# Performance work log

Hardware: AMD Instinct MI355X
Metric: run time of the kernel (lower is better)

## Reference

```python
import jax, jax.numpy as jnp
import numpy as np

G = 2            # num_codevector_groups
C = 320          # num_codevectors_per_group
VQ_DIM = 256     # codevector_dim
HID = 512        # conv_dimensions[-1]
TAU = 2.0


def setup_inputs() -> dict:
    key = jax.random.key(0)
    k1, k2, k3, k4 = jax.random.split(key, 4)
    B, S = 16, 2048
    x = jax.random.normal(k1, (B, S, HID), dtype=jnp.float32)
    # iid Gumbel(0,1) noise, same shape as flattened logits [B*S*G, C]
    u = jax.random.uniform(k2, (B * S * G, C), dtype=jnp.float32, minval=1e-6, maxval=1.0 - 1e-6)
    gumbel = -jnp.log(-jnp.log(u))
    Wq = jax.random.normal(k3, (G * C, HID), dtype=jnp.float32) * (1.0 / np.sqrt(HID))
    bq = jnp.zeros((G * C,), dtype=jnp.float32)
    codevectors = jax.random.uniform(k4, (1, G * C, VQ_DIM // G), dtype=jnp.float32)
    return {"x": x, "gumbel": gumbel, "Wq": Wq, "bq": bq, "codevectors": codevectors}


def reference(x, gumbel, Wq, bq, codevectors):
    B, S, H = x.shape
    N = B * S
    logits = jnp.einsum('bsh,gh->bsg', x, Wq) + bq          # [B, S, G*C]
    logits = logits.reshape(N * G, C)

    # hard gumbel-softmax (training path) with straight-through estimator
    y_soft = jax.nn.softmax((logits + gumbel) / TAU, axis=-1)
    idx = jnp.argmax(y_soft, axis=-1)
    y_hard = jax.nn.one_hot(idx, C, dtype=y_soft.dtype)
    probs = y_hard + y_soft - jax.lax.stop_gradient(y_soft)  # [N*G, C]

    # perplexity from plain softmax of logits (no gumbel noise), masked_token_idx=None
    soft_probs = jax.nn.softmax(logits.reshape(N, G, C), axis=-1)
    mean_p = soft_probs.mean(axis=0)                          # [G, C]
    perplexity = jnp.exp(-jnp.sum(mean_p * jnp.log(mean_p + 1e-7), axis=-1)).sum()

    # weighted sum over codes per group == einsum (same math as broadcast*sum in torch)
    cv = codevectors.reshape(G, C, VQ_DIM // G)               # [G, C, d]
    sel = jnp.einsum('ngc,gcd->ngd', probs.reshape(N, G, C), cv)
    selected_codes = sel.reshape(B, S, VQ_DIM)
    return selected_codes, perplexity
```

## Files before the change

### kernel.cpp

```cpp
#include <hip/hip_runtime.h>
#include <hip/hip_fp16.h>

#define HID 512
#define GC  640
#define CC  320
#define GG  2
#define DHALF 128
#define MARGIN 0.004f
#define FB 4

typedef __attribute__((ext_vector_type(8))) _Float16 half8;
typedef __attribute__((ext_vector_type(4))) float float4v;

__device__ __forceinline__ void gload16(const void* g, void* l) {
    __builtin_amdgcn_global_load_lds(
        (const __attribute__((address_space(1))) void*)(unsigned long long)g,
        (__attribute__((address_space(3))) void*)(unsigned)(unsigned long long)l,
        16, 0, 0);
}

__global__ __launch_bounds__(256) void zero_misc(float* meanAcc, int* cnt) {
    for (int i = threadIdx.x; i < GC; i += 256) meanAcc[i] = 0.f;
    if (threadIdx.x < 2) cnt[threadIdx.x] = 0;
}

__global__ __launch_bounds__(256) void convert_f16(
    const float* __restrict__ in, unsigned short* __restrict__ out, int n8)
{
    int i = blockIdx.x * 256 + threadIdx.x;
    if (i >= n8) return;
    const float4* p = (const float4*)in + (size_t)i * 2;
    float4 v0 = p[0], v1 = p[1];
    float f[8] = {v0.x, v0.y, v0.z, v0.w, v1.x, v1.y, v1.z, v1.w};
    unsigned r[4];
#pragma unroll
    for (int j = 0; j < 4; ++j) {
        __half2 hh = __float22half2_rn(make_float2(f[2*j], f[2*j+1]));
        r[j] = __builtin_bit_cast(unsigned, hh);
    }
    uint4 o = {r[0], r[1], r[2], r[3]};
    *(uint4*)(out + (size_t)i * 8) = o;
}

__global__ __launch_bounds__(256) void gemm_f16(
    const unsigned short* __restrict__ Xh,
    const unsigned short* __restrict__ Wh,
    const float* __restrict__ bq,
    float* __restrict__ L)
{
    __shared__ __align__(16) unsigned short As[128 * 32];
    __shared__ __align__(16) unsigned short Bs[128 * 32];
    const int tid  = threadIdx.x;
    const int lane = tid & 63;
    const int wid  = tid >> 6;
    const int wr   = wid >> 1, wc = wid & 1;
    const int brow = blockIdx.x * 128;
    const int bcol = blockIdx.y * 128;

    float4v acc[4][4] = {};

    const int chunk = (wid * 2) * 64 + lane;
    const int rowA0 = (chunk >> 2);
    const int k8A0  = (chunk & 3) * 8;
    const int chunk1 = (wid * 2 + 1) * 64 + lane;
    const int rowA1 = (chunk1 >> 2);
    const int k8A1  = (chunk1 & 3) * 8;

    for (int k0 = 0; k0 < HID; k0 += 32) {
        gload16(Xh + (size_t)(brow + rowA0) * HID + k0 + k8A0, &As[(wid * 2 + 0) * 512]);
        gload16(Xh + (size_t)(brow + rowA1) * HID + k0 + k8A1, &As[(wid * 2 + 1) * 512]);
        gload16(Wh + (size_t)(bcol + rowA0) * HID + k0 + k8A0, &Bs[(wid * 2 + 0) * 512]);
        gload16(Wh + (size_t)(bcol + rowA1) * HID + k0 + k8A1, &Bs[(wid * 2 + 1) * 512]);
        __syncthreads();
        half8 a[4], b[4];
#pragma unroll
        for (int t = 0; t < 4; ++t) {
            a[t] = *(const half8*)(const void*)&As[(wr * 64 + t * 16 + (lane & 15)) * 32 + (lane >> 4) * 8];
            b[t] = *(const half8*)(const void*)&Bs[(wc * 64 + t * 16 + (lane & 15)) * 32 + (lane >> 4) * 8];
        }
#pragma unroll
        for (int mt = 0; mt < 4; ++mt)
#pragma unroll
            for (int nt = 0; nt < 4; ++nt)
                acc[mt][nt] = __builtin_amdgcn_mfma_f32_16x16x32_f16(a[mt], b[nt], acc[mt][nt], 0, 0, 0);
        __syncthreads();
    }
#pragma unroll
    for (int mt = 0; mt < 4; ++mt) {
#pragma unroll
        for (int nt = 0; nt < 4; ++nt) {
            int col = bcol + wc * 64 + nt * 16 + (lane & 15);
            float bias = bq[col];
#pragma unroll
            for (int r = 0; r < 4; ++r) {
                int row = brow + wr * 64 + mt * 16 + (lane >> 4) * 4 + r;
                L[(size_t)row * GC + col] = acc[mt][nt][r] + bias;
            }
        }
    }
}

__global__ __launch_bounds__(512) void postproc(
    const float* __restrict__ L, const float* __restrict__ gum,
    const float* __restrict__ cv, float* __restrict__ out,
    float* __restrict__ meanAcc, int* __restrict__ cnt,
    int* __restrict__ flags0, int* __restrict__ flags1, int tok0)
{
    __shared__ float smean[GC];
    for (int i = threadIdx.x; i < GC; i += 512) smean[i] = 0.f;
    __syncthreads();

    const int lane = threadIdx.x & 63;
    const int wid  = threadIdx.x >> 6;
    const int g    = wid >> 2;
    const int lq   = lane & 15;
    const int tq   = lane >> 4;
    const int c0   = lq * 20;
    int* flagsg = g ? flags1 : flags0;

    float macc[20];
#pragma unroll
    for (int j = 0; j < 20; ++j) macc[j] = 0.f;

    for (int it = 0; it < 4; ++it) {
        const int tloc  = blockIdx.x * 64 + (wid & 3) * 16 + it * 4 + tq;
        const int tglob = tok0 + tloc;
        const float* lrow = L   + (size_t)tloc * GC + g * CC + c0;
        const float* grow = gum + ((size_t)tglob * GG + g) * CC + c0;

        float le[20], ve[20];
#pragma unroll
        for (int jj = 0; jj < 5; ++jj) {
            float4 lv = *(const float4*)(lrow + jj * 4);
            float4 gv = *(const float4*)(grow + jj * 4);
            le[jj*4+0] = lv.x; le[jj*4+1] = lv.y; le[jj*4+2] = lv.z; le[jj*4+3] = lv.w;
            ve[jj*4+0] = lv.x + gv.x; ve[jj*4+1] = lv.y + gv.y;
            ve[jj*4+2] = lv.z + gv.z; ve[jj*4+3] = lv.w + gv.w;
        }
        float s = 0.f;
#pragma unroll
        for (int j = 0; j < 20; ++j) { le[j] = __expf(le[j]); s += le[j]; }
        float b = ve[0]; int bi = c0; float s2 = -3.0e38f;
#pragma unroll
        for (int j = 1; j < 20; ++j) {
            float v = ve[j];
            if (v > b) { s2 = b; b = v; bi = c0 + j; }
            else if (v > s2) s2 = v;
        }
#pragma unroll
        for (int m = 1; m < 16; m <<= 1) {
            float os  = __shfl_xor(s,  m, 64);
            float ob  = __shfl_xor(b,  m, 64);
            int   obi = __shfl_xor(bi, m, 64);
            float os2 = __shfl_xor(s2, m, 64);
            s += os;
            if (ob > b || (ob == b && obi < bi)) { s2 = fmaxf(os2, b); b = ob; bi = obi; }
            else                                 { s2 = fmaxf(s2, ob); }
        }
        float inv = 1.f / s;
#pragma unroll
        for (int j = 0; j < 20; ++j) macc[j] += le[j] * inv;

        if (lq == 0 && (b - s2) < MARGIN) {
            int p = atomicAdd(&cnt[g], 1);
            flagsg[p] = tglob;
        }
        const float* cvp = cv + ((size_t)(g * CC + bi)) * DHALF + lq * 8;
        float4 c0v = *(const float4*)cvp;
        float4 c1v = *(const float4*)(cvp + 4);
        float* op = out + (size_t)tglob * 256 + g * DHALF + lq * 8;
        *(float4*)op       = c0v;
        *(float4*)(op + 4) = c1v;
    }
#pragma unroll
    for (int j = 0; j < 20; ++j) {
        macc[j] += __shfl_xor(macc[j], 16, 64);
        macc[j] += __shfl_xor(macc[j], 32, 64);
    }
    if (lane < 16) {
#pragma unroll
        for (int j = 0; j < 20; ++j)
            atomicAdd(&smean[g * CC + c0 + j], macc[j]);
    }
    __syncthreads();
    for (int i = threadIdx.x; i < GC; i += 512)
        atomicAdd(&meanAcc[i], smean[i]);
}

__global__ __launch_bounds__(320) void fixup(
    const float* __restrict__ X, const float* __restrict__ W,
    const float* __restrict__ bq, const float* __restrict__ gum,
    const float* __restrict__ cv, float* __restrict__ out,
    const int* __restrict__ flags0, const int* __restrict__ flags1,
    const int* __restrict__ cnt)
{
    __shared__ float xs[FB][HID];
    __shared__ float vals[FB][CC];
    __shared__ int stok[FB];
    const int tid = threadIdx.x;
    const int n0 = cnt[0], n1 = cnt[1];
    const int nb0 = (n0 + FB - 1) / FB;
    const int nb1 = (n1 + FB - 1) / FB;

    for (int bb = blockIdx.x; bb < nb0 + nb1; bb += gridDim.x) {
        const int g    = (bb < nb0) ? 0 : 1;
        const int lb   = (bb < nb0) ? bb : bb - nb0;
        const int n    = g ? n1 : n0;
        const int* fl  = g ? flags1 : flags0;
        const int r0   = lb * FB;
        const int nr   = (n - r0 < FB) ? (n - r0) : FB;

        if (tid < FB) {
            int idx = r0 + tid;
            if (idx >= n) idx = n - 1;
            stok[tid] = fl[idx];
        }
        __syncthreads();
        for (int i = tid; i < FB * (HID / 4); i += 320) {
            int r = i >> 7, k4 = i & 127;
            *(float4*)&xs[r][k4 * 4] = *(const float4*)(X + (size_t)stok[r] * HID + k4 * 4);
        }
        __syncthreads();

        {
            const int c = tid;
            if (c < CC) {
                const float* wr = W + (size_t)(g * CC + c) * HID;
                float acc[FB];
#pragma unroll
                for (int r = 0; r < FB; ++r) acc[r] = 0.f;
                for (int k4 = 0; k4 < HID / 4; ++k4) {
                    float4 w4 = *(const float4*)(wr + k4 * 4);
#pragma unroll
                    for (int r = 0; r < FB; ++r) {
                        float4 xv = *(const float4*)&xs[r][k4 * 4];
                        acc[r] = fmaf(xv.x, w4.x, acc[r]);
                        acc[r] = fmaf(xv.y, w4.y, acc[r]);
                        acc[r] = fmaf(xv.z, w4.z, acc[r]);
                        acc[r] = fmaf(xv.w, w4.w, acc[r]);
                    }
                }
                float bias = bq[g * CC + c];
#pragma unroll
                for (int r = 0; r < FB; ++r)
                    vals[r][c] = acc[r] + bias + gum[((size_t)stok[r] * GG + g) * CC + c];
            }
        }
        __syncthreads();

        const int lane = tid & 63;
        const int wv   = tid >> 6;
        if (wv < FB) {
            const int r = wv;
            if (r < nr) {
                float b = -3.0e38f; int bi = 0;
#pragma unroll
                for (int j = 0; j < 5; ++j) {
                    int c = lane + j * 64;
                    float v = vals[r][c];
                    if (v > b || (v == b && c < bi)) { b = v; bi = c; }
                }
#pragma unroll
                for (int m = 32; m; m >>= 1) {
                    float ob = __shfl_xor(b, m, 64);
                    int  obi = __shfl_xor(bi, m, 64);
                    if (ob > b || (ob == b && obi < bi)) { b = ob; bi = obi; }
                }
                int tok = stok[r];
                float2 cvv = *(const float2*)(cv + ((size_t)(g * CC + bi)) * DHALF + lane * 2);
                *(float2*)(out + (size_t)tok * 256 + g * DHALF + lane * 2) = cvv;
            }
        }
        __syncthreads();
    }
}

__global__ __launch_bounds__(256) void perpk(
    const float* __restrict__ meanAcc, float* __restrict__ outp, int ntot)
{
    __shared__ float red0[256];
    __shared__ float red1[256];
    const float invn = 1.f / (float)ntot;
    float h0 = 0.f, h1 = 0.f;
    for (int c = threadIdx.x; c < CC; c += 256) {
        float p0 = meanAcc[c]      * invn;
        float p1 = meanAcc[CC + c] * invn;
        h0 -= p0 * logf(p0 + 1e-7f);
        h1 -= p1 * logf(p1 + 1e-7f);
    }
    red0[threadIdx.x] = h0; red1[threadIdx.x] = h1;
    __syncthreads();
    for (int s = 128; s; s >>= 1) {
        if (threadIdx.x < (unsigned)s) {
            red0[threadIdx.x] += red0[threadIdx.x + s];
            red1[threadIdx.x] += red1[threadIdx.x + s];
        }
        __syncthreads();
    }
    if (threadIdx.x == 0) outp[0] = expf(red0[0]) + expf(red1[0]);
}

extern "C" void kernel_launch(void* const* d_in, const int* in_sizes, int n_in,
                              void* d_out, int out_size, void* d_ws, size_t ws_size,
                              hipStream_t stream) {
    const float* x      = (const float*)d_in[0];
    const float* gumbel = (const float*)d_in[1];
    const float* Wq     = (const float*)d_in[2];
    const float* bq     = (const float*)d_in[3];
    const float* cv     = (const float*)d_in[4];
    float* out = (float*)d_out;

    const int NT = in_sizes[0] / HID;

    char* wsc = (char*)d_ws;
    float* meanAcc = (float*)wsc;
    int*   cnt     = (int*)(wsc + 2560);
    int*   flags0  = (int*)(wsc + 4096);
    int*   flags1  = (int*)(wsc + 135168);
    unsigned short* Wh = (unsigned short*)(wsc + 266240);
    const size_t base = 921600;

    size_t avail = ws_size > base ? ws_size - base : 0;
    long maxTok = (long)(avail / 3584);
    int CH = (int)((maxTok / 128) * 128);
    if (CH > NT) CH = NT;
    if (CH < 128) CH = 128;
    unsigned short* Xh = (unsigned short*)(wsc + base);
    float* Lbuf = (float*)(wsc + base + (size_t)CH * 1024);

    zero_misc<<<1, 256, 0, stream>>>(meanAcc, cnt);
    convert_f16<<<(GC * HID / 8 + 255) / 256, 256, 0, stream>>>(Wq, Wh, GC * HID / 8);

    for (int t0 = 0; t0 < NT; t0 += CH) {
        int cur = NT - t0 < CH ? NT - t0 : CH;
        int n8 = cur * HID / 8;
        convert_f16<<<(n8 + 255) / 256, 256, 0, stream>>>(
            x + (size_t)t0 * HID, Xh, n8);
        dim3 ggrid(cur / 128, GC / 128);
        gemm_f16<<<ggrid, 256, 0, stream>>>(Xh, Wh, bq, Lbuf);
        postproc<<<cur / 64, 512, 0, stream>>>(Lbuf, gumbel, cv, out, meanAcc, cnt,
                                               flags0, flags1, t0);
    }
    fixup<<<256, 320, 0, stream>>>(x, Wq, bq, gumbel, cv, out, flags0, flags1, cnt);
    perpk<<<1, 256, 0, stream>>>(meanAcc, out + (size_t)out_size - 1, NT);
}
```

Baseline: 141.4 us.

## Fuse x conversion, GEMM and gumbel postprocessing into one kernel per token-group tile

Replaces the separate x-to-fp16 conversion, tiled GEMM writing fp32 logits, and postprocessing kernel with one fused kernel. Each workgroup owns 128 tokens and one codebook group, converts x to fp16 in registers while staging it in LDS, computes all 320 logits per token with MFMA, and runs softmax, argmax and the perplexity accumulation directly from the accumulators. This removes the global round trip of the fp16 x copy and the full fp32 logits buffer, plus extra launches. In exchange, x is read and converted twice (once per group), register pressure rises with 20 accumulator tiles, and per-iteration syncs leave no load/compute overlap.

```diff
diff --git a/kernel.cpp b/kernel.cpp
--- a/kernel.cpp
+++ b/kernel.cpp
@@ -42,110 +42,88 @@
     *(uint4*)(out + (size_t)i * 8) = o;
 }
 
-__global__ __launch_bounds__(256) void gemm_f16(
-    const unsigned short* __restrict__ Xh,
-    const unsigned short* __restrict__ Wh,
-    const float* __restrict__ bq,
-    float* __restrict__ L)
+__global__ __launch_bounds__(512, 4) void fused(
+    const float* __restrict__ X, const unsigned short* __restrict__ Wh,
+    const float* __restrict__ bq, const float* __restrict__ gum,
+    const float* __restrict__ cv, float* __restrict__ out,
+    float* __restrict__ meanAcc, int* __restrict__ cnt,
+    int* __restrict__ flags0, int* __restrict__ flags1)
 {
     __shared__ __align__(16) unsigned short As[128 * 32];
-    __shared__ __align__(16) unsigned short Bs[128 * 32];
+    __shared__ __align__(16) unsigned short Bs[384 * 32];
+    __shared__ float bqs[CC];
+    __shared__ float smean[CC];
+
     const int tid  = threadIdx.x;
     const int lane = tid & 63;
     const int wid  = tid >> 6;
-    const int wr   = wid >> 1, wc = wid & 1;
-    const int brow = blockIdx.x * 128;
-    const int bcol = blockIdx.y * 128;
-
-    float4v acc[4][4] = {};
-
-    const int chunk = (wid * 2) * 64 + lane;
-    const int rowA0 = (chunk >> 2);
-    const int k8A0  = (chunk & 3) * 8;
-    const int chunk1 = (wid * 2 + 1) * 64 + lane;
-    const int rowA1 = (chunk1 >> 2);
-    const int k8A1  = (chunk1 & 3) * 8;
+    const int lq   = lane & 15;
+    const int q    = lane >> 4;
+
+    int bid = blockIdx.x;
+    int nwg = gridDim.x;
+    int swz = ((nwg & 7) == 0) ? (bid & 7) * (nwg >> 3) + (bid >> 3) : bid;
+    const int g    = swz & 1;
+    const int tok0 = (swz >> 1) * 128;
+    int* flagsg = g ? flags1 : flags0;
+
+    for (int i = tid; i < CC; i += 512) { bqs[i] = bq[g * CC + i]; smean[i] = 0.f; }
+
+    float4v acc[20];
+#pragma unroll
+    for (int j = 0; j < 20; ++j) acc[j] = (float4v){0.f, 0.f, 0.f, 0.f};
+
+    const int arow = tid >> 2, aslot = tid & 3;
+    const float* xsrc = X + (size_t)(tok0 + arow) * HID + aslot * 8;
 
     for (int k0 = 0; k0 < HID; k0 += 32) {
-        gload16(Xh + (size_t)(brow + rowA0) * HID + k0 + k8A0, &As[(wid * 2 + 0) * 512]);
-        gload16(Xh + (size_t)(brow + rowA1) * HID + k0 + k8A1, &As[(wid * 2 + 1) * 512]);
-        gload16(Wh + (size_t)(bcol + rowA0) * HID + k0 + k8A0, &Bs[(wid * 2 + 0) * 512]);
-        gload16(Wh + (size_t)(bcol + rowA1) * HID + k0 + k8A1, &Bs[(wid * 2 + 1) * 512]);
-        __syncthreads();
-        half8 a[4], b[4];
-#pragma unroll
-        for (int t = 0; t < 4; ++t) {
-            a[t] = *(const half8*)(const void*)&As[(wr * 64 + t * 16 + (lane & 15)) * 32 + (lane >> 4) * 8];
-            b[t] = *(const half8*)(const void*)&Bs[(wc * 64 + t * 16 + (lane & 15)) * 32 + (lane >> 4) * 8];
-        }
-#pragma unroll
-        for (int mt = 0; mt < 4; ++mt)
-#pragma unroll
-            for (int nt = 0; nt < 4; ++nt)
-                acc[mt][nt] = __builtin_amdgcn_mfma_f32_16x16x32_f16(a[mt], b[nt], acc[mt][nt], 0, 0, 0);
-        __syncthreads();
-    }
-#pragma unroll
-    for (int mt = 0; mt < 4; ++mt) {
-#pragma unroll
-        for (int nt = 0; nt < 4; ++nt) {
-            int col = bcol + wc * 64 + nt * 16 + (lane & 15);
-            float bias = bq[col];
-#pragma unroll
-            for (int r = 0; r < 4; ++r) {
-                int row = brow + wr * 64 + mt * 16 + (lane >> 4) * 4 + r;
-                L[(size_t)row * GC + col] = acc[mt][nt][r] + bias;
-            }
-        }
-    }
-}
-
-__global__ __launch_bounds__(512) void postproc(
-    const float* __restrict__ L, const float* __restrict__ gum,
-    const float* __restrict__ cv, float* __restrict__ out,
-    float* __restrict__ meanAcc, int* __restrict__ cnt,
-    int* __restrict__ flags0, int* __restrict__ flags1, int tok0)
-{
-    __shared__ float smean[GC];
-    for (int i = threadIdx.x; i < GC; i += 512) smean[i] = 0.f;
-    __syncthreads();
-
-    const int lane = threadIdx.x & 63;
-    const int wid  = threadIdx.x >> 6;
-    const int g    = wid >> 2;
-    const int lq   = lane & 15;
-    const int tq   = lane >> 4;
-    const int c0   = lq * 20;
-    int* flagsg = g ? flags1 : flags0;
+        float4 xa = *(const float4*)(xsrc + k0);
+        float4 xb = *(const float4*)(xsrc + k0 + 4);
+        half8 h;
+        h[0] = (_Float16)xa.x; h[1] = (_Float16)xa.y;
+        h[2] = (_Float16)xa.z; h[3] = (_Float16)xa.w;
+        h[4] = (_Float16)xb.x; h[5] = (_Float16)xb.y;
+        h[6] = (_Float16)xb.z; h[7] = (_Float16)xb.w;
+        *(half8*)&As[arow * 32 + aslot * 8] = h;
+#pragma unroll
+        for (int ii = 0; ii < 3; ++ii) {
+            const int iss = wid * 3 + ii;
+            int e  = iss * 64 + lane;
+            int br = e >> 2; if (br > 319) br = 319;
+            int bs = e & 3;
+            gload16(Wh + ((size_t)(g * CC + br)) * HID + k0 + bs * 8,
+                    &Bs[iss * 512]);
+        }
+        __syncthreads();
+        half8 a = *(const half8*)&As[(wid * 16 + lq) * 32 + q * 8];
+#pragma unroll
+        for (int j = 0; j < 20; ++j) {
+            half8 b = *(const half8*)&Bs[(j * 16 + lq) * 32 + q * 8];
+            acc[j] = __builtin_amdgcn_mfma_f32_16x16x32_f16(a, b, acc[j], 0, 0, 0);
+        }
+        __syncthreads();
+    }
 
     float macc[20];
 #pragma unroll
     for (int j = 0; j < 20; ++j) macc[j] = 0.f;
 
-    for (int it = 0; it < 4; ++it) {
-        const int tloc  = blockIdx.x * 64 + (wid & 3) * 16 + it * 4 + tq;
-        const int tglob = tok0 + tloc;
-        const float* lrow = L   + (size_t)tloc * GC + g * CC + c0;
-        const float* grow = gum + ((size_t)tglob * GG + g) * CC + c0;
-
-        float le[20], ve[20];
-#pragma unroll
-        for (int jj = 0; jj < 5; ++jj) {
-            float4 lv = *(const float4*)(lrow + jj * 4);
-            float4 gv = *(const float4*)(grow + jj * 4);
-            le[jj*4+0] = lv.x; le[jj*4+1] = lv.y; le[jj*4+2] = lv.z; le[jj*4+3] = lv.w;
-            ve[jj*4+0] = lv.x + gv.x; ve[jj*4+1] = lv.y + gv.y;
-            ve[jj*4+2] = lv.z + gv.z; ve[jj*4+3] = lv.w + gv.w;
-        }
+#pragma unroll
+    for (int r = 0; r < 4; ++r) {
+        const int rowL  = wid * 16 + q * 4 + r;
+        const int tglob = tok0 + rowL;
+        const float* grow = gum + ((size_t)tglob * GG + g) * CC;
+        float le[20];
         float s = 0.f;
-#pragma unroll
-        for (int j = 0; j < 20; ++j) { le[j] = __expf(le[j]); s += le[j]; }
-        float b = ve[0]; int bi = c0; float s2 = -3.0e38f;
-#pragma unroll
-        for (int j = 1; j < 20; ++j) {
-            float v = ve[j];
-            if (v > b) { s2 = b; b = v; bi = c0 + j; }
-            else if (v > s2) s2 = v;
+        float b = -3.0e38f; int bi = 0; float s2 = -3.0e38f;
+#pragma unroll
+        for (int j = 0; j < 20; ++j) {
+            const int c = j * 16 + lq;
+            float lg = acc[j][r] + bqs[c];
+            float v  = lg + grow[c];
+            if (v > b)       { s2 = b; b = v; bi = c; }
+            else if (v > s2) { s2 = v; }
+            le[j] = __expf(lg); s += le[j];
         }
 #pragma unroll
         for (int m = 1; m < 16; m <<= 1) {
@@ -180,11 +158,11 @@
     if (lane < 16) {
 #pragma unroll
         for (int j = 0; j < 20; ++j)
-            atomicAdd(&smean[g * CC + c0 + j], macc[j]);
+            atomicAdd(&smean[j * 16 + lq], macc[j]);
     }
     __syncthreads();
-    for (int i = threadIdx.x; i < GC; i += 512)
-        atomicAdd(&meanAcc[i], smean[i]);
+    for (int i = tid; i < CC; i += 512)
+        atomicAdd(&meanAcc[g * CC + i], smean[i]);
 }
 
 __global__ __launch_bounds__(320) void fixup(
@@ -318,29 +296,14 @@
     int*   flags0  = (int*)(wsc + 4096);
     int*   flags1  = (int*)(wsc + 135168);
     unsigned short* Wh = (unsigned short*)(wsc + 266240);
-    const size_t base = 921600;
-
-    size_t avail = ws_size > base ? ws_size - base : 0;
-    long maxTok = (long)(avail / 3584);
-    int CH = (int)((maxTok / 128) * 128);
-    if (CH > NT) CH = NT;
-    if (CH < 128) CH = 128;
-    unsigned short* Xh = (unsigned short*)(wsc + base);
-    float* Lbuf = (float*)(wsc + base + (size_t)CH * 1024);
 
     zero_misc<<<1, 256, 0, stream>>>(meanAcc, cnt);
     convert_f16<<<(GC * HID / 8 + 255) / 256, 256, 0, stream>>>(Wq, Wh, GC * HID / 8);
 
-    for (int t0 = 0; t0 < NT; t0 += CH) {
-        int cur = NT - t0 < CH ? NT - t0 : CH;
-        int n8 = cur * HID / 8;
-        convert_f16<<<(n8 + 255) / 256, 256, 0, stream>>>(
-            x + (size_t)t0 * HID, Xh, n8);
-        dim3 ggrid(cur / 128, GC / 128);
-        gemm_f16<<<ggrid, 256, 0, stream>>>(Xh, Wh, bq, Lbuf);
-        postproc<<<cur / 64, 512, 0, stream>>>(Lbuf, gumbel, cv, out, meanAcc, cnt,
-                                               flags0, flags1, t0);
-    }
+    const int nwg = (NT / 128) * 2;
+    fused<<<nwg, 512, 0, stream>>>(x, Wh, bq, gumbel, cv, out,
+                                   meanAcc, cnt, flags0, flags1);
+
     fixup<<<256, 320, 0, stream>>>(x, Wq, bq, gumbel, cv, out, flags0, flags1, cnt);
     perpk<<<1, 256, 0, stream>>>(meanAcc, out + (size_t)out_size - 1, NT);
 }
```

New measurement: 116.8 us. 17.4% less time.
